# Kernel optimization log

Hardware: AMD Instinct MI355X
Metric: run time of the kernel (lower is better)

The kernel has to match this reference:

```python
import jax, jax.numpy as jnp
import numpy as np

N = 128            # codeword length (power of 2)
LIST = 8           # SCL list size
L2 = 2 * LIST      # decoders kept during path expansion
STAGES = 7         # log2(N)
LLR_MAX = 30.0
BATCH = 2048
FROZEN_POS = np.arange(N // 2)
FROZEN_IND = np.zeros(N, dtype=bool)
FROZEN_IND[FROZEN_POS] = True
INFO_POS = np.setdiff1d(np.arange(N), FROZEN_POS)


def _cn_op(x, y):
    # min-sum boxplus with LLR clipping
    x = jnp.clip(x, -LLR_MAX, LLR_MAX)
    y = jnp.clip(y, -LLR_MAX, LLR_MAX)
    return jnp.sign(x) * jnp.sign(y) * jnp.minimum(jnp.abs(x), jnp.abs(y))


def _vn_op(x, y, u):
    return (1.0 - 2.0 * u) * x + y


def _leaf(state, i):
    # Update single bit i across all 2L decoders, update path metrics,
    # and for info bits sort + duplicate the best L paths.
    uhat, llr, pm, ptr, bidx = state
    frozen = bool(FROZEN_IND[i])
    if not frozen:
        # set bit=1 for the upper half of decoders (path expansion)
        u_slice = uhat[:, :, 0, i]
        u_slice = u_slice.at[bidx[:, None], ptr[:, LIST:]].set(1.0)
        uhat = uhat.at[:, :, 0, i].set(u_slice)
    # path metric update, Eq.(10) of Stimming et al.
    u = jnp.take_along_axis(uhat[:, :, 0, i], ptr, axis=1)
    l = jnp.clip(jnp.take_along_axis(llr[:, :, 0, i], ptr, axis=1), -LLR_MAX, LLR_MAX)
    pm = pm + jax.nn.softplus(-(1.0 - 2.0 * u) * l)
    if not frozen:
        order = jnp.argsort(pm, axis=-1)
        pm = jnp.take_along_axis(pm, order, axis=1)
        ptr = jnp.take_along_axis(ptr, order, axis=1)
        lo = ptr[:, :LIST]
        up = ptr[:, LIST:]
        uhat = uhat.at[bidx[:, None], up].set(uhat[bidx[:, None], lo])
        llr = llr.at[bidx[:, None], up].set(llr[bidx[:, None], lo])
        pm = pm.at[:, LIST:].set(pm[:, :LIST])
    return (uhat, llr, pm, ptr, bidx)


def _decode(state, start, length):
    # recursive SCL tree traversal over contiguous index block [start, start+length)
    if length == 1:
        return _leaf(state, start)
    s = int(np.log2(length))
    h = length // 2
    uhat, llr, pm, ptr, bidx = state
    lsl = slice(start, start + h)
    rsl = slice(start + h, start + length)
    # f (check-node) update -> left child
    f = _cn_op(llr[:, :, s, lsl], llr[:, :, s, rsl])
    llr = llr.at[:, :, s - 1, lsl].set(f)
    uhat, llr, pm, ptr, bidx = _decode((uhat, llr, pm, ptr, bidx), start, h)
    # g (variable-node) update -> right child
    g = _vn_op(llr[:, :, s, lsl], llr[:, :, s, rsl], uhat[:, :, s - 1, lsl])
    llr = llr.at[:, :, s - 1, rsl].set(g)
    uhat, llr, pm, ptr, bidx = _decode((uhat, llr, pm, ptr, bidx), start + h, h)
    # combine partial sums: left XOR right, right pass-through
    ul = uhat[:, :, s - 1, lsl]
    ur = uhat[:, :, s - 1, rsl]
    ux = ul + ur - 2.0 * ul * ur  # XOR for {0,1} values (differentiable form)
    uhat = uhat.at[:, :, s, start:start + length].set(jnp.concatenate([ux, ur], axis=-1))
    return (uhat, llr, pm, ptr, bidx)


def setup_inputs() -> dict:
    key = jax.random.key(0)
    inputs = 2.0 * jax.random.normal(key, (BATCH, N), dtype=jnp.float32)
    return {"inputs": inputs}


def reference(inputs):
    bs = inputs.shape[0]
    llr_ch = -inputs.astype(jnp.float32)  # logits -> LLR sign convention
    uhat = jnp.zeros((bs, L2, STAGES + 1, N), jnp.float32)
    llr = jnp.zeros((bs, L2, STAGES + 1, N), jnp.float32)
    llr = llr.at[:, :, STAGES, :].set(llr_ch[:, None, :])
    pm = jnp.zeros((bs, L2), jnp.float32)
    pm = pm.at[:, 1:LIST].set(LLR_MAX).at[:, LIST + 1:].set(LLR_MAX)
    ptr = jnp.tile(jnp.arange(L2)[None, :], (bs, 1))
    bidx = jnp.arange(bs)
    uhat, llr, pm, ptr, _ = _decode((uhat, llr, pm, ptr, bidx), 0, N)
    # final sort and de-permutation of the list dimension
    order = jnp.argsort(pm, axis=-1)
    pm = jnp.take_along_axis(pm, order, axis=1)
    ptr = jnp.take_along_axis(ptr, order, axis=1)
    uhat = uhat[bidx[:, None], ptr]
    cand = jnp.argmin(pm, axis=-1)
    c_hat = uhat[bidx, cand, 0, :]       # [bs, n] best codeword estimate
    return c_hat[:, INFO_POS]            # [bs, k] info bits
```

## Files before the change

### kernel.cpp

```cpp
#include <hip/hip_runtime.h>
#include <math.h>

#define LMAX 30.0f
typedef unsigned long long ull;
typedef unsigned int u32;

__device__ __forceinline__ float clip30(float x) { return fminf(fmaxf(x, -LMAX), LMAX); }
__device__ __forceinline__ float cnop(float x, float y) {
    x = clip30(x); y = clip30(y);
    const float m = fminf(fabsf(x), fabsf(y));
    const unsigned sg = (__float_as_uint(x) ^ __float_as_uint(y)) & 0x80000000u;
    return __uint_as_float(__float_as_uint(m) | sg);
}

#define SWZI(x, PAT) __builtin_amdgcn_ds_swizzle((x), (PAT))
#define SWZF(x, PAT) __int_as_float(__builtin_amdgcn_ds_swizzle(__float_as_int(x), (PAT)))

template<int CTRL>
__device__ __forceinline__ int dppi(int x) {
    return __builtin_amdgcn_update_dpp(x, x, CTRL, 0xF, 0xF, false);
}
template<int CTRL>
__device__ __forceinline__ float dppf(float x) {
    return __int_as_float(dppi<CTRL>(__float_as_int(x)));
}
#define CTL_XOR8 0x128
#define CTL_XOR2 0x4E
#define CTL_XOR1 0xB1

#if __has_builtin(__builtin_amdgcn_permlane32_swap)
typedef int v2i_ __attribute__((ext_vector_type(2)));
__device__ __forceinline__ int swap32i(int x) {
    v2i_ r = __builtin_amdgcn_permlane32_swap(x, x, false, false);
    return (r[0] != x) ? r[0] : r[1];
}
#else
__device__ __forceinline__ int swap32i(int x) {
    int a = x, b = x;
    asm volatile("v_permlane32_swap_b32 %0, %1" : "+v"(a), "+v"(b));
    return (a != x) ? a : b;
}
#endif
#if __has_builtin(__builtin_amdgcn_permlane16_swap)
typedef int v2j_ __attribute__((ext_vector_type(2)));
__device__ __forceinline__ int swap16i(int x) {
    v2j_ r = __builtin_amdgcn_permlane16_swap(x, x, false, false);
    return (r[0] != x) ? r[0] : r[1];
}
#else
__device__ __forceinline__ int swap16i(int x) { return SWZI(x, 0x401F); }
#endif
__device__ __forceinline__ float swap32f(float x) { return __int_as_float(swap32i(__float_as_int(x))); }
__device__ __forceinline__ float swap16f(float x) { return __int_as_float(swap16i(__float_as_int(x))); }

__device__ __forceinline__ float gfb(float v, int a) {
    return __int_as_float(__builtin_amdgcn_ds_bpermute(a, __float_as_int(v)));
}
__device__ __forceinline__ ull bperm64b(ull v, int a) {
    const int lo = __builtin_amdgcn_ds_bpermute(a, (int)(u32)v);
    const int hi = __builtin_amdgcn_ds_bpermute(a, (int)(u32)(v >> 32));
    return ((ull)(u32)hi << 32) | (u32)lo;
}

__device__ __forceinline__ u32 enc2(u32 w)  { w ^= (w >> 1) & 0x1u; return w; }
__device__ __forceinline__ u32 enc4(u32 w)  { w ^= (w >> 1) & 0x5u; w ^= (w >> 2) & 0x3u; return w; }
__device__ __forceinline__ u32 enc8(u32 w)  { w ^= (w >> 1) & 0x55u; w ^= (w >> 2) & 0x33u;
                                              w ^= (w >> 4) & 0x0fu; return w; }
__device__ __forceinline__ u32 enc16(u32 w) { w ^= (w >> 1) & 0x5555u; w ^= (w >> 2) & 0x3333u;
                                              w ^= (w >> 4) & 0x0f0fu; w ^= (w >> 8) & 0x00ffu; return w; }
__device__ __forceinline__ u32 enc32(u32 w) { w ^= (w >> 1) & 0x55555555u; w ^= (w >> 2) & 0x33333333u;
                                              w ^= (w >> 4) & 0x0f0f0f0fu; w ^= (w >> 8) & 0x00ff00ffu;
                                              w ^= (w >> 16) & 0x0000ffffu; return w; }

#define F6_() { _Pragma("unroll") for (int k = 0; k < 8; ++k) S5[k] = cnop(C[k], C[k + 8]); }
#define G6_(II) { const u32 ub = enc32((u32)(uh >> ((II) - 96))); \
    _Pragma("unroll") for (int k = 0; k < 8; ++k) { \
        const int u = (ub >> (p + 4 * k)) & 1; \
        S5[k] = u ? (C[k + 8] - C[k]) : (C[k + 8] + C[k]); } }
#define F5_() { _Pragma("unroll") for (int k = 0; k < 4; ++k) S4[k] = cnop(S5[k], S5[k + 4]); }
#define G5_(II) { const u32 ub = enc16((u32)(uh >> ((II) - 80)) & 0xffffu); \
    _Pragma("unroll") for (int k = 0; k < 4; ++k) { \
        const int u = (ub >> (p + 4 * k)) & 1; \
        S4[k] = u ? (S5[k + 4] - S5[k]) : (S5[k + 4] + S5[k]); } }
#define F4_() { S3[0] = cnop(S4[0], S4[2]); S3[1] = cnop(S4[1], S4[3]); }
#define G4_(II) { const u32 ub = enc8((u32)(uh >> ((II) - 72)) & 0xffu); \
    _Pragma("unroll") for (int k = 0; k < 2; ++k) { \
        const int u = (ub >> (p + 4 * k)) & 1; \
        S3[k] = u ? (S4[k + 2] - S4[k]) : (S4[k + 2] + S4[k]); } }
#define REPL2(v0) { \
    const float t1_ = swap16f(v0); \
    const float lo_ = (p & 1) ? t1_ : (v0); \
    const float hi_ = (p & 1) ? (v0) : t1_; \
    const float lo2_ = swap32f(lo_); \
    const float hi2_ = swap32f(hi_); \
    R2[0] = (p < 2) ? lo_ : lo2_; R2[1] = (p < 2) ? hi_ : hi2_; \
    R2[2] = (p < 2) ? lo2_ : lo_; R2[3] = (p < 2) ? hi2_ : hi_; }
#define F3R_() { const float v0_ = cnop(S3[0], S3[1]); REPL2(v0_); }
#define G3R_(II) { const u32 ub = enc4((u32)(uh >> ((II) - 68)) & 0xfu); \
    const int u = (ub >> p) & 1; \
    const float v0_ = u ? (S3[1] - S3[0]) : (S3[1] + S3[0]); REPL2(v0_); }
#define F2_() { R1[0] = cnop(R2[0], R2[2]); R1[1] = cnop(R2[1], R2[3]); }
#define G2_(II) { const u32 ub = enc2((u32)(uh >> ((II) - 66)) & 3u); \
    R1[0] = (ub & 1) ? (R2[2] - R2[0]) : (R2[2] + R2[0]); \
    R1[1] = (ub & 2) ? (R2[3] - R2[1]) : (R2[3] + R2[1]); }

#define LEAF_(II, L0, DOCLONE) { \
    uh |= upBit << ((II) - 64); \
    const float l_ = clip30(L0); \
    const float tail_ = log1pf(expf(-fabsf(l_))); \
    pm += (isUp ? fmaxf(l_, 0.0f) : fmaxf(-l_, 0.0f)) + tail_; \
    int r_ = 0; \
    { \
        const u32 pmB = __float_as_uint(pm); \
        _Pragma("unroll") \
        for (int k = 0; k < 4; ++k) { \
            const u32 pmj = (u32)__builtin_amdgcn_ds_bpermute(A[k], __float_as_int(pm)); \
            r_ += ((pmj < pmB) || (pmj == pmB && (4 * p + k) < pos)) ? 1 : 0; \
        } \
    } \
    r_ += swap32i(r_); \
    r_ += swap16i(r_); \
    rFinal = r_; \
    if (DOCLONE) { \
        const int inv_ = __builtin_amdgcn_ds_permute(((r_ ^ swp8) | gbase) << 2, pos); \
        const int p8_ = dppi<CTL_XOR8>(inv_); \
        const int ga_ = ((needP ? p8_ : inv_) | gbase) << 2; \
        pm = gfb(pm, ga_); \
        uh = bperm64b(uh, ga_); \
        if ((((II) >> 0) & 1) == 0) { R1[0] = gfb(R1[0], ga_); R1[1] = gfb(R1[1], ga_); } \
        if ((((II) >> 1) & 1) == 0) { _Pragma("unroll") for (int e = 0; e < 4; ++e) \
                                      R2[e] = gfb(R2[e], ga_); } \
        if ((((II) >> 2) & 1) == 0) { _Pragma("unroll") for (int e = 0; e < 2; ++e) \
                                      S3[e] = gfb(S3[e], ga_); } \
        if ((((II) >> 3) & 1) == 0) { _Pragma("unroll") for (int e = 0; e < 4; ++e) \
                                      S4[e] = gfb(S4[e], ga_); } \
        if ((((II) >> 4) & 1) == 0) { _Pragma("unroll") for (int e = 0; e < 8; ++e) \
                                      S5[e] = gfb(S5[e], ga_); } \
    } \
}

__global__ __launch_bounds__(64) void scl_kernel(const float* __restrict__ in,
                                                 float* __restrict__ out) {
    __shared__ float ch6s[64];
    const int b = blockIdx.x;
    const int lane = threadIdx.x;
    const int pos = lane & 15;
    const int p = lane >> 4;
    const int gbase = lane & 48;
    const bool isUp = (lane & 8) != 0;
    const ull upBit = (ull)((lane >> 3) & 1);
    const int swp8 = (lane & 32) >> 2;
    const bool needP = (((lane >> 3) ^ (lane >> 5)) & 1) != 0;

    const float a = -in[(size_t)b * 128 + lane];
    const float c = -in[(size_t)b * 128 + 64 + lane];
    ch6s[lane] = a + c;
    __syncthreads();

    float C[16];
    #pragma unroll
    for (int k = 0; k < 16; ++k) C[k] = ch6s[p + 4 * k];

    float v = cnop(a, c);
    { const float o = swap32f(v);            v = (lane & 32) ? (o + v) : cnop(v, o); }
    { const float o = swap16f(v);            v = (lane & 16) ? (o + v) : cnop(v, o); }
    { const float o = dppf<CTL_XOR8>(v);     v = (lane & 8)  ? (o + v) : cnop(v, o); }
    { const float o = SWZF(v, 0x101F);       v = (lane & 4)  ? (o + v) : cnop(v, o); }
    { const float o = dppf<CTL_XOR2>(v);     v = (lane & 2)  ? (o + v) : cnop(v, o); }
    { const float o = dppf<CTL_XOR1>(v);     v = (lane & 1)  ? (o + v) : cnop(v, o); }
    const float spf = fmaxf(-clip30(v), 0.0f) + log1pf(expf(-fabsf(clip30(v))));
    float pm = (pos == 0 || pos == 8) ? 0.0f : LMAX;
    #pragma unroll
    for (int j = 0; j < 64; ++j)
        pm += __uint_as_float((u32)__builtin_amdgcn_readlane(__float_as_int(spf), j));

    int A[4];
    #pragma unroll
    for (int k = 0; k < 4; ++k) A[k] = ((4 * p + k) | gbase) << 2;

    float S5[8], S4[4], S3[2], R2[4], R1[2];
    ull uh = 0;
    int rFinal = 0;

    #pragma unroll 1
    for (int ie = 64; ie < 128; ie += 2) {
        {
            const int ii = ie;
            const int t = __builtin_ctz(ii);
            switch (t) {
                case 1: { G2_(ii); } break;
                case 2: { G3R_(ii); F2_(); } break;
                case 3: { G4_(ii); F3R_(); F2_(); } break;
                case 4: { G5_(ii); F4_(); F3R_(); F2_(); } break;
                case 5: { G6_(ii); F5_(); F4_(); F3R_(); F2_(); } break;
                default: { F6_(); F5_(); F4_(); F3R_(); F2_(); } break;
            }
            const float l0 = cnop(R1[0], R1[1]);
            LEAF_(ii, l0, 1);
        }
        {
            const int ii = ie + 1;
            const int ug = (int)((uh >> (ii - 65)) & 1ULL);
            const float l0 = ug ? (R1[1] - R1[0]) : (R1[1] + R1[0]);
            LEAF_(ii, l0, (ii != 127));
        }
    }

    const ull m = __ballot(rFinal == 0);
    const int bl = (int)__builtin_ctzll(m);
    const u32 wlo = (u32)__builtin_amdgcn_readlane((int)(u32)uh, bl);
    const u32 whi = (u32)__builtin_amdgcn_readlane((int)(u32)(uh >> 32), bl);
    const ull w = ((ull)whi << 32) | wlo;
    out[(size_t)b * 64 + lane] = (float)((w >> lane) & 1ULL);
}

extern "C" void kernel_launch(void* const* d_in, const int* in_sizes, int n_in,
                              void* d_out, int out_size, void* d_ws, size_t ws_size,
                              hipStream_t stream) {
    (void)n_in; (void)out_size; (void)d_ws; (void)ws_size;
    const float* in = (const float*)d_in[0];
    float* out = (float*)d_out;
    const int batch = in_sizes[0] / 128;
    scl_kernel<<<dim3(batch), dim3(64), 0, stream>>>(in, out);
}
```

Baseline: 64.02 us.

## Pack two codewords per wavefront with 32 lanes each

Remaps the decoder so each 64-lane wavefront decodes two codewords, one per half-wave, with 16 paths times 2 lanes per codeword. Each lane now holds twice as many LLR values per stage (C[32], S5[16], etc.), the rank computation uses 8 comparisons instead of 4 plus one fewer cross-lane swap, and the grid is halved. This removes the 32-lane swap traffic and amortizes per-wave serial latency across two codewords, at the cost of more registers and more per-lane arithmetic and bpermutes during cloning. It assumes an even batch size.

```diff
diff --git a/kernel.cpp b/kernel.cpp
--- a/kernel.cpp
+++ b/kernel.cpp
@@ -28,19 +28,6 @@
 #define CTL_XOR2 0x4E
 #define CTL_XOR1 0xB1
 
-#if __has_builtin(__builtin_amdgcn_permlane32_swap)
-typedef int v2i_ __attribute__((ext_vector_type(2)));
-__device__ __forceinline__ int swap32i(int x) {
-    v2i_ r = __builtin_amdgcn_permlane32_swap(x, x, false, false);
-    return (r[0] != x) ? r[0] : r[1];
-}
-#else
-__device__ __forceinline__ int swap32i(int x) {
-    int a = x, b = x;
-    asm volatile("v_permlane32_swap_b32 %0, %1" : "+v"(a), "+v"(b));
-    return (a != x) ? a : b;
-}
-#endif
 #if __has_builtin(__builtin_amdgcn_permlane16_swap)
 typedef int v2j_ __attribute__((ext_vector_type(2)));
 __device__ __forceinline__ int swap16i(int x) {
@@ -50,7 +37,6 @@
 #else
 __device__ __forceinline__ int swap16i(int x) { return SWZI(x, 0x401F); }
 #endif
-__device__ __forceinline__ float swap32f(float x) { return __int_as_float(swap32i(__float_as_int(x))); }
 __device__ __forceinline__ float swap16f(float x) { return __int_as_float(swap16i(__float_as_int(x))); }
 
 __device__ __forceinline__ float gfb(float v, int a) {
@@ -72,33 +58,31 @@
                                               w ^= (w >> 4) & 0x0f0f0f0fu; w ^= (w >> 8) & 0x00ff00ffu;
                                               w ^= (w >> 16) & 0x0000ffffu; return w; }
 
-#define F6_() { _Pragma("unroll") for (int k = 0; k < 8; ++k) S5[k] = cnop(C[k], C[k + 8]); }
+#define F6_() { _Pragma("unroll") for (int k = 0; k < 16; ++k) S5[k] = cnop(C[k], C[k + 16]); }
 #define G6_(II) { const u32 ub = enc32((u32)(uh >> ((II) - 96))); \
+    _Pragma("unroll") for (int k = 0; k < 16; ++k) { \
+        const int u = (ub >> (q + 2 * k)) & 1; \
+        S5[k] = u ? (C[k + 16] - C[k]) : (C[k + 16] + C[k]); } }
+#define F5_() { _Pragma("unroll") for (int k = 0; k < 8; ++k) S4[k] = cnop(S5[k], S5[k + 8]); }
+#define G5_(II) { const u32 ub = enc16((u32)(uh >> ((II) - 80)) & 0xffffu); \
     _Pragma("unroll") for (int k = 0; k < 8; ++k) { \
-        const int u = (ub >> (p + 4 * k)) & 1; \
-        S5[k] = u ? (C[k + 8] - C[k]) : (C[k + 8] + C[k]); } }
-#define F5_() { _Pragma("unroll") for (int k = 0; k < 4; ++k) S4[k] = cnop(S5[k], S5[k + 4]); }
-#define G5_(II) { const u32 ub = enc16((u32)(uh >> ((II) - 80)) & 0xffffu); \
+        const int u = (ub >> (q + 2 * k)) & 1; \
+        S4[k] = u ? (S5[k + 8] - S5[k]) : (S5[k + 8] + S5[k]); } }
+#define F4_() { _Pragma("unroll") for (int k = 0; k < 4; ++k) S3[k] = cnop(S4[k], S4[k + 4]); }
+#define G4_(II) { const u32 ub = enc8((u32)(uh >> ((II) - 72)) & 0xffu); \
     _Pragma("unroll") for (int k = 0; k < 4; ++k) { \
-        const int u = (ub >> (p + 4 * k)) & 1; \
-        S4[k] = u ? (S5[k + 4] - S5[k]) : (S5[k + 4] + S5[k]); } }
-#define F4_() { S3[0] = cnop(S4[0], S4[2]); S3[1] = cnop(S4[1], S4[3]); }
-#define G4_(II) { const u32 ub = enc8((u32)(uh >> ((II) - 72)) & 0xffu); \
-    _Pragma("unroll") for (int k = 0; k < 2; ++k) { \
-        const int u = (ub >> (p + 4 * k)) & 1; \
-        S3[k] = u ? (S4[k + 2] - S4[k]) : (S4[k + 2] + S4[k]); } }
-#define REPL2(v0) { \
-    const float t1_ = swap16f(v0); \
-    const float lo_ = (p & 1) ? t1_ : (v0); \
-    const float hi_ = (p & 1) ? (v0) : t1_; \
-    const float lo2_ = swap32f(lo_); \
-    const float hi2_ = swap32f(hi_); \
-    R2[0] = (p < 2) ? lo_ : lo2_; R2[1] = (p < 2) ? hi_ : hi2_; \
-    R2[2] = (p < 2) ? lo2_ : lo_; R2[3] = (p < 2) ? hi2_ : hi_; }
-#define F3R_() { const float v0_ = cnop(S3[0], S3[1]); REPL2(v0_); }
+        const int u = (ub >> (q + 2 * k)) & 1; \
+        S3[k] = u ? (S4[k + 4] - S4[k]) : (S4[k + 4] + S4[k]); } }
+#define REPL2_(t0, t1) { \
+    const float P0_ = swap16f(t0), P1_ = swap16f(t1); \
+    R2[0] = q ? P0_ : (t0); R2[1] = q ? (t0) : P0_; \
+    R2[2] = q ? P1_ : (t1); R2[3] = q ? (t1) : P1_; }
+#define F3R_() { const float a0_ = cnop(S3[0], S3[2]); \
+                 const float a1_ = cnop(S3[1], S3[3]); REPL2_(a0_, a1_); }
 #define G3R_(II) { const u32 ub = enc4((u32)(uh >> ((II) - 68)) & 0xfu); \
-    const int u = (ub >> p) & 1; \
-    const float v0_ = u ? (S3[1] - S3[0]) : (S3[1] + S3[0]); REPL2(v0_); }
+    const int u0 = (ub >> q) & 1, u1 = (ub >> (q + 2)) & 1; \
+    const float a0_ = u0 ? (S3[2] - S3[0]) : (S3[2] + S3[0]); \
+    const float a1_ = u1 ? (S3[3] - S3[1]) : (S3[3] + S3[1]); REPL2_(a0_, a1_); }
 #define F2_() { R1[0] = cnop(R2[0], R2[2]); R1[1] = cnop(R2[1], R2[3]); }
 #define G2_(II) { const u32 ub = enc2((u32)(uh >> ((II) - 66)) & 3u); \
     R1[0] = (ub & 1) ? (R2[2] - R2[0]) : (R2[2] + R2[0]); \
@@ -113,72 +97,92 @@
     { \
         const u32 pmB = __float_as_uint(pm); \
         _Pragma("unroll") \
-        for (int k = 0; k < 4; ++k) { \
-            const u32 pmj = (u32)__builtin_amdgcn_ds_bpermute(A[k], __float_as_int(pm)); \
-            r_ += ((pmj < pmB) || (pmj == pmB && (4 * p + k) < pos)) ? 1 : 0; \
+        for (int k = 0; k < 8; ++k) { \
+            const u32 pmj = (u32)__builtin_amdgcn_ds_bpermute(A0 + 4 * k, __float_as_int(pm)); \
+            r_ += ((pmj < pmB) || (pmj == pmB && (idx0 + k) < pos)) ? 1 : 0; \
         } \
     } \
-    r_ += swap32i(r_); \
     r_ += swap16i(r_); \
     rFinal = r_; \
     if (DOCLONE) { \
-        const int inv_ = __builtin_amdgcn_ds_permute(((r_ ^ swp8) | gbase) << 2, pos); \
+        const int inv_ = __builtin_amdgcn_ds_permute((r_ | gbase) << 2, pos); \
         const int p8_ = dppi<CTL_XOR8>(inv_); \
-        const int ga_ = ((needP ? p8_ : inv_) | gbase) << 2; \
+        const int ga_ = ((isUp ? p8_ : inv_) | gbase) << 2; \
         pm = gfb(pm, ga_); \
         uh = bperm64b(uh, ga_); \
         if ((((II) >> 0) & 1) == 0) { R1[0] = gfb(R1[0], ga_); R1[1] = gfb(R1[1], ga_); } \
         if ((((II) >> 1) & 1) == 0) { _Pragma("unroll") for (int e = 0; e < 4; ++e) \
                                       R2[e] = gfb(R2[e], ga_); } \
-        if ((((II) >> 2) & 1) == 0) { _Pragma("unroll") for (int e = 0; e < 2; ++e) \
+        if ((((II) >> 2) & 1) == 0) { _Pragma("unroll") for (int e = 0; e < 4; ++e) \
                                       S3[e] = gfb(S3[e], ga_); } \
-        if ((((II) >> 3) & 1) == 0) { _Pragma("unroll") for (int e = 0; e < 4; ++e) \
+        if ((((II) >> 3) & 1) == 0) { _Pragma("unroll") for (int e = 0; e < 8; ++e) \
                                       S4[e] = gfb(S4[e], ga_); } \
-        if ((((II) >> 4) & 1) == 0) { _Pragma("unroll") for (int e = 0; e < 8; ++e) \
+        if ((((II) >> 4) & 1) == 0) { _Pragma("unroll") for (int e = 0; e < 16; ++e) \
                                       S5[e] = gfb(S5[e], ga_); } \
     } \
 }
 
+#define RLF(x, J) __uint_as_float((u32)__builtin_amdgcn_readlane(__float_as_int(x), (J)))
+
 __global__ __launch_bounds__(64) void scl_kernel(const float* __restrict__ in,
                                                  float* __restrict__ out) {
-    __shared__ float ch6s[64];
-    const int b = blockIdx.x;
+    __shared__ float chS[128];
     const int lane = threadIdx.x;
+    const int w = lane & 31;
+    const int d = lane >> 5;
     const int pos = lane & 15;
-    const int p = lane >> 4;
+    const int q = (lane >> 4) & 1;
     const int gbase = lane & 48;
+    const int dbase = lane & 32;
     const bool isUp = (lane & 8) != 0;
     const ull upBit = (ull)((lane >> 3) & 1);
-    const int swp8 = (lane & 32) >> 2;
-    const bool needP = (((lane >> 3) ^ (lane >> 5)) & 1) != 0;
-
-    const float a = -in[(size_t)b * 128 + lane];
-    const float c = -in[(size_t)b * 128 + 64 + lane];
-    ch6s[lane] = a + c;
+    const int idx0 = q << 3;
+    const int A0 = (dbase | (q << 3)) << 2;
+
+    const size_t base = ((size_t)blockIdx.x * 2 + d) * 128;
+    const float a1 = -in[base + w],      c1 = -in[base + 64 + w];
+    const float a2 = -in[base + 32 + w], c2 = -in[base + 96 + w];
+    chS[d * 64 + w] = a1 + c1;
+    chS[d * 64 + 32 + w] = a2 + c2;
     __syncthreads();
-
-    float C[16];
+    float C[32];
     #pragma unroll
-    for (int k = 0; k < 16; ++k) C[k] = ch6s[p + 4 * k];
-
-    float v = cnop(a, c);
-    { const float o = swap32f(v);            v = (lane & 32) ? (o + v) : cnop(v, o); }
-    { const float o = swap16f(v);            v = (lane & 16) ? (o + v) : cnop(v, o); }
-    { const float o = dppf<CTL_XOR8>(v);     v = (lane & 8)  ? (o + v) : cnop(v, o); }
-    { const float o = SWZF(v, 0x101F);       v = (lane & 4)  ? (o + v) : cnop(v, o); }
-    { const float o = dppf<CTL_XOR2>(v);     v = (lane & 2)  ? (o + v) : cnop(v, o); }
-    { const float o = dppf<CTL_XOR1>(v);     v = (lane & 1)  ? (o + v) : cnop(v, o); }
-    const float spf = fmaxf(-clip30(v), 0.0f) + log1pf(expf(-fabsf(clip30(v))));
-    float pm = (pos == 0 || pos == 8) ? 0.0f : LMAX;
-    #pragma unroll
-    for (int j = 0; j < 64; ++j)
-        pm += __uint_as_float((u32)__builtin_amdgcn_readlane(__float_as_int(spf), j));
-
-    int A[4];
-    #pragma unroll
-    for (int k = 0; k < 4; ++k) A[k] = ((4 * p + k) | gbase) << 2;
-
-    float S5[8], S4[4], S3[2], R2[4], R1[2];
+    for (int k = 0; k < 32; ++k) C[k] = chS[d * 64 + q + 2 * k];
+
+    float v1 = cnop(a1, c1), v2 = cnop(a2, c2);
+    { const float n1 = cnop(v1, v2); v2 = v1 + v2; v1 = n1; }
+    { const float o1 = swap16f(v1), o2 = swap16f(v2);
+      v1 = (w & 16) ? (o1 + v1) : cnop(v1, o1);
+      v2 = (w & 16) ? (o2 + v2) : cnop(v2, o2); }
+    { const float o1 = dppf<CTL_XOR8>(v1), o2 = dppf<CTL_XOR8>(v2);
+      v1 = (w & 8) ? (o1 + v1) : cnop(v1, o1);
+      v2 = (w & 8) ? (o2 + v2) : cnop(v2, o2); }
+    { const float o1 = SWZF(v1, 0x101F), o2 = SWZF(v2, 0x101F);
+      v1 = (w & 4) ? (o1 + v1) : cnop(v1, o1);
+      v2 = (w & 4) ? (o2 + v2) : cnop(v2, o2); }
+    { const float o1 = dppf<CTL_XOR2>(v1), o2 = dppf<CTL_XOR2>(v2);
+      v1 = (w & 2) ? (o1 + v1) : cnop(v1, o1);
+      v2 = (w & 2) ? (o2 + v2) : cnop(v2, o2); }
+    { const float o1 = dppf<CTL_XOR1>(v1), o2 = dppf<CTL_XOR1>(v2);
+      v1 = (w & 1) ? (o1 + v1) : cnop(v1, o1);
+      v2 = (w & 1) ? (o2 + v2) : cnop(v2, o2); }
+    const float sp1 = fmaxf(-clip30(v1), 0.0f) + log1pf(expf(-fabsf(clip30(v1))));
+    const float sp2 = fmaxf(-clip30(v2), 0.0f) + log1pf(expf(-fabsf(clip30(v2))));
+
+    float pm = ((pos == 0) || (pos == 8)) ? 0.0f : LMAX;
+    if (lane < 32) {
+        #pragma unroll
+        for (int j = 0; j < 32; ++j) pm += RLF(sp1, j);
+        #pragma unroll
+        for (int j = 0; j < 32; ++j) pm += RLF(sp2, j);
+    } else {
+        #pragma unroll
+        for (int j = 32; j < 64; ++j) pm += RLF(sp1, j);
+        #pragma unroll
+        for (int j = 32; j < 64; ++j) pm += RLF(sp2, j);
+    }
+
+    float S5[16], S4[8], S3[4], R2[4], R1[2];
     ull uh = 0;
     int rFinal = 0;
 
@@ -207,11 +211,11 @@
     }
 
     const ull m = __ballot(rFinal == 0);
-    const int bl = (int)__builtin_ctzll(m);
-    const u32 wlo = (u32)__builtin_amdgcn_readlane((int)(u32)uh, bl);
-    const u32 whi = (u32)__builtin_amdgcn_readlane((int)(u32)(uh >> 32), bl);
-    const ull w = ((ull)whi << 32) | wlo;
-    out[(size_t)b * 64 + lane] = (float)((w >> lane) & 1ULL);
+    const int bl = dbase + (int)__builtin_ctz((u32)(m >> dbase));
+    const ull uhB = bperm64b(uh, bl << 2);
+    const size_t ob = ((size_t)blockIdx.x * 2 + d) * 64;
+    out[ob + w] = (float)((uhB >> w) & 1ULL);
+    out[ob + 32 + w] = (float)((uhB >> (w + 32)) & 1ULL);
 }
 
 extern "C" void kernel_launch(void* const* d_in, const int* in_sizes, int n_in,
@@ -221,5 +225,5 @@
     const float* in = (const float*)d_in[0];
     float* out = (float*)d_out;
     const int batch = in_sizes[0] / 128;
-    scl_kernel<<<dim3(batch), dim3(64), 0, stream>>>(in, out);
-}
+    scl_kernel<<<dim3(batch / 2), dim3(64), 0, stream>>>(in, out);
+}
```

Result: faster. 62.35 us (-2.6%).
